# Performance work log

Measured on AMD Instinct MI355X. Metric: run time of the kernel, lower is better.

The kernel has to match this reference:

```python
import jax, jax.numpy as jnp
import numpy as np
from jax import lax

R = 8  # REGION_NUM_

def _avgpool3(x):
    # AvgPool2d(kernel=H-2*(H//3), stride=H//3) -> exactly 3x3 spatial output
    H = x.shape[2]
    s = H // 3
    k = H - 2 * s
    y = lax.reduce_window(x, 0.0, lax.add, (1, 1, k, k), (1, 1, s, s), 'VALID')
    return y / float(k * k)

def _hist_drconv(x, hist, wa, ba, wb, bb, out_ch):
    # x: [B,Cin,H,W], hist: [B,R,H,W]
    B, Cin, H, W = x.shape
    p = _avgpool3(x)                                                     # [B,Cin,3,3]
    h = jax.nn.sigmoid(jnp.einsum('bchw,oc->bohw', p, wa) + ba[None, :, None, None])  # [B,R*R,3,3]
    hg = h.reshape(B, R, R, 3, 3)
    wbg = wb.reshape(R, Cin * out_ch, R)                                 # grouped 1x1 conv, groups=R
    kern = jnp.einsum('brchw,roc->brohw', hg, wbg) + bb.reshape(1, R, Cin * out_ch, 1, 1)
    ki = kern.reshape(B, R * out_ch, Cin, 3, 3)                          # per-sample dynamic kernels
    def per_sample(xi, kb):
        # xi: [Cin,H,W], kb: [R*out,Cin,3,3] -> [R*out,H,W]
        return lax.conv_general_dilated(xi[None], kb, (1, 1), [(1, 1), (1, 1)])[0]
    y = jax.vmap(per_sample)(x, ki)                                      # [B,R*out,H,W]
    y = y.reshape(B, R, out_ch, H, W)
    # asign_index: one-hot of argmax over regions, select-sum
    mask = jax.nn.one_hot(jnp.argmax(hist, axis=1), R, axis=1, dtype=y.dtype)  # [B,R,H,W]
    return (y * mask[:, :, None]).sum(axis=1)                            # [B,out,H,W]

def _bn_relu(y, g, b, m, v):
    scale = (g / jnp.sqrt(v + 1e-5))[None, :, None, None]
    return jax.nn.relu((y - m[None, :, None, None]) * scale + b[None, :, None, None])

def setup_inputs() -> dict:
    key = jax.random.key(0)
    ks = jax.random.split(key, 20)
    B, Cin, Cmid, Cout, H = 8, 8, 8, 8, 256
    f32 = jnp.float32
    d = {}
    d['x'] = jax.random.normal(ks[0], (B, Cin, H, H), f32)
    d['histmap'] = jax.random.uniform(ks[1], (B, R, H, H), dtype=f32)
    d['w1a'] = jax.random.normal(ks[2], (R * R, Cin), f32) * 0.1
    d['b1a'] = jax.random.normal(ks[3], (R * R,), f32) * 0.1
    d['w1b'] = jax.random.normal(ks[4], (R * Cin * Cmid, R), f32) * 0.1
    d['b1b'] = jax.random.normal(ks[5], (R * Cin * Cmid,), f32) * 0.1
    d['g1'] = jax.random.uniform(ks[6], (Cmid,), dtype=f32) + 0.5
    d['be1'] = jax.random.normal(ks[7], (Cmid,), f32) * 0.1
    d['m1'] = jax.random.normal(ks[8], (Cmid,), f32) * 0.1
    d['v1'] = jax.random.uniform(ks[9], (Cmid,), dtype=f32) + 0.5
    d['w2a'] = jax.random.normal(ks[10], (R * R, Cmid), f32) * 0.1
    d['b2a'] = jax.random.normal(ks[11], (R * R,), f32) * 0.1
    d['w2b'] = jax.random.normal(ks[12], (R * Cmid * Cout, R), f32) * 0.1
    d['b2b'] = jax.random.normal(ks[13], (R * Cmid * Cout,), f32) * 0.1
    d['g2'] = jax.random.uniform(ks[14], (Cout,), dtype=f32) + 0.5
    d['be2'] = jax.random.normal(ks[15], (Cout,), f32) * 0.1
    d['m2'] = jax.random.normal(ks[16], (Cout,), f32) * 0.1
    d['v2'] = jax.random.uniform(ks[17], (Cout,), dtype=f32) + 0.5
    return d

def reference(x, histmap, w1a, b1a, w1b, b1b, g1, be1, m1, v1,
              w2a, b2a, w2b, b2b, g2, be2, m2, v2):
    y = _hist_drconv(x, histmap, w1a, b1a, w1b, b1b, 8)
    y = _bn_relu(y, g1, be1, m1, v1)
    y = _hist_drconv(y, histmap, w2a, b2a, w2b, b2b, 8)
    return _bn_relu(y, g2, be2, m2, v2)
```

## Files before the change

### kernel.cpp

```cpp
#include <hip/hip_runtime.h>
#include <math.h>


#define HWPX 65536
#define HDIM 256

typedef __fp16 h2 __attribute__((ext_vector_type(2)));

#if defined(__has_builtin) && __has_builtin(__builtin_amdgcn_fdot2)
__device__ __forceinline__ float fdot2(h2 a, h2 b, float c) {
  return __builtin_amdgcn_fdot2(a, b, c, false);
}
#else
__device__ __forceinline__ float fdot2(h2 a, h2 b, float c) {
  return c + (float)a[0] * (float)b[0] + (float)a[1] * (float)b[1];
}
#endif

union UH { uint u; h2 h; };
union U4H { uint4 u4; h2 h[4]; };

__global__ __launch_bounds__(256) void prep_kernel(const float* __restrict__ x,
                                                   const float* __restrict__ hist,
                                                   float* __restrict__ rs,
                                                   uint* __restrict__ xh,
                                                   unsigned char* __restrict__ regmap) {
  int bid = blockIdx.x;
  int wave = threadIdx.x >> 6, lane = threadIdx.x & 63;
  if (bid < 2048) {
    int cp = bid & 3, rg = (bid >> 2) & 63, b = bid >> 8;
    int row = rg * 4 + wave;
    const float* pa = x + ((size_t)(b * 8 + 2 * cp) * HWPX) + row * HDIM + lane * 4;
    const float4 va = *(const float4*)pa;
    const float4 vb = *(const float4*)(pa + HWPX);
    U4H pk;
    pk.h[0] = __builtin_amdgcn_cvt_pkrtz(va.x, vb.x);
    pk.h[1] = __builtin_amdgcn_cvt_pkrtz(va.y, vb.y);
    pk.h[2] = __builtin_amdgcn_cvt_pkrtz(va.z, vb.z);
    pk.h[3] = __builtin_amdgcn_cvt_pkrtz(va.w, vb.w);
    *(uint4*)(xh + (size_t)(b * 4 + cp) * HWPX + row * HDIM + lane * 4) = pk.u4;
    float a0 = 0.f, a1 = 0.f, a2 = 0.f, b0 = 0.f, b1 = 0.f, b2 = 0.f;
#pragma unroll
    for (int p = 0; p < 4; p++) {
      int px = lane * 4 + p;
      float fa = (&va.x)[p], fb = (&vb.x)[p];
      if (px <= 85)  { a0 += fa; b0 += fb; }
      if (px >= 85 && px <= 170) { a1 += fa; b1 += fb; }
      if (px >= 170) { a2 += fa; b2 += fb; }
    }
#pragma unroll
    for (int off = 32; off >= 1; off >>= 1) {
      a0 += __shfl_xor(a0, off); a1 += __shfl_xor(a1, off); a2 += __shfl_xor(a2, off);
      b0 += __shfl_xor(b0, off); b1 += __shfl_xor(b1, off); b2 += __shfl_xor(b2, off);
    }
    if (lane == 0) {
      float* qa = rs + ((size_t)(b * 8 + 2 * cp) * 256 + row) * 3;
      qa[0] = a0; qa[1] = a1; qa[2] = a2;
      float* qb = qa + 768;
      qb[0] = b0; qb[1] = b1; qb[2] = b2;
    }
  } else {
    int bid2 = bid - 2048;
    int b = bid2 >> 6, rg = bid2 & 63;
    int row = rg * 4 + wave;
    int x0 = lane * 4;
    const float* hp = hist + (size_t)b * 8 * HWPX + row * HDIM + x0;
    float4 hv[8];
#pragma unroll
    for (int r = 0; r < 8; r++) hv[r] = *(const float4*)(hp + (size_t)r * HWPX);
    uchar4 rg4;
#pragma unroll
    for (int p = 0; p < 4; p++) {
      float best = (&hv[0].x)[p];
      int reg = 0;
#pragma unroll
      for (int r = 1; r < 8; r++) {
        float q = (&hv[r].x)[p];
        if (q > best) { best = q; reg = r; }
      }
      (&rg4.x)[p] = (unsigned char)reg;
    }
    *(uchar4*)(regmap + (size_t)b * HWPX + row * HDIM + x0) = rg4;
  }
}

__global__ __launch_bounds__(256) void rowsum_h_kernel(const uint* __restrict__ yh,
                                                       float* __restrict__ rs) {
  int bid = blockIdx.x;
  int cp = bid & 3, rg = (bid >> 2) & 63, b = bid >> 8;
  int wave = threadIdx.x >> 6, lane = threadIdx.x & 63;
  int row = rg * 4 + wave;
  uint4 u = *(const uint4*)(yh + (size_t)(b * 4 + cp) * HWPX + row * HDIM + lane * 4);
  float a0 = 0.f, a1 = 0.f, a2 = 0.f, b0 = 0.f, b1 = 0.f, b2 = 0.f;
#pragma unroll
  for (int p = 0; p < 4; p++) {
    UH w; w.u = (&u.x)[p];
    float fa = (float)w.h[0], fb = (float)w.h[1];
    int px = lane * 4 + p;
    if (px <= 85)  { a0 += fa; b0 += fb; }
    if (px >= 85 && px <= 170) { a1 += fa; b1 += fb; }
    if (px >= 170) { a2 += fa; b2 += fb; }
  }
#pragma unroll
  for (int off = 32; off >= 1; off >>= 1) {
    a0 += __shfl_xor(a0, off); a1 += __shfl_xor(a1, off); a2 += __shfl_xor(a2, off);
    b0 += __shfl_xor(b0, off); b1 += __shfl_xor(b1, off); b2 += __shfl_xor(b2, off);
  }
  if (lane == 0) {
    float* qa = rs + ((size_t)(b * 8 + 2 * cp) * 256 + row) * 3;
    qa[0] = a0; qa[1] = a1; qa[2] = a2;
    float* qb = qa + 768;
    qb[0] = b0; qb[1] = b1; qb[2] = b2;
  }
}

template <int LAYER>
__global__ __launch_bounds__(256) void conv_kernel(
    const uint* __restrict__ xh, const unsigned char* __restrict__ regmap,
    const float* __restrict__ rs,
    const float* __restrict__ wa, const float* __restrict__ ba,
    const float* __restrict__ wb, const float* __restrict__ bb,
    const float* __restrict__ g, const float* __restrict__ be,
    const float* __restrict__ m, const float* __restrict__ v,
    uint* __restrict__ outh, float* __restrict__ outf) {
  __shared__ uint KsU[8 * 292];
  __shared__ float pp[72][3];
  __shared__ float pP[8][9];
  __shared__ float hh[576];
  __shared__ float bns[8], bnsh[8];

  int bid = blockIdx.x;
  int b = bid & 7;
  int rg = bid >> 3;
  int wave = threadIdx.x >> 6, lane = threadIdx.x & 63;
  int row = rg * 4 + wave;
  int x0 = lane * 4;
  int t = threadIdx.x;

  if (t < 216) {
    int u = t / 3, part = t - 3 * (t / 3);
    int c = u / 9, ij = u % 9, i = ij / 3, j = ij % 3;
    int r0 = 85 * i + part * 29;
    int cnt = (part == 2) ? 28 : 29;
    const float* q = rs + ((size_t)(b * 8 + c) * 256 + r0) * 3 + j;
    float s = 0.f;
    for (int k = 0; k < cnt; k++) s += q[k * 3];
    pp[u][part] = s;
  }
  if (t >= 248) {
    int oc = t - 248;
    float s = g[oc] * rsqrtf(v[oc] + 1e-5f);
    bns[oc] = s;
    bnsh[oc] = be[oc] - m[oc] * s;
  }
  __syncthreads();
  if (t < 72) pP[t / 9][t % 9] = (pp[t][0] + pp[t][1] + pp[t][2]) * (1.f / 7396.f);
  __syncthreads();
  for (int u = t; u < 576; u += 256) {
    int o = u / 9, ij = u - o * 9;
    float z = ba[o];
#pragma unroll
    for (int c = 0; c < 8; c++) z += pP[c][ij] * wa[o * 8 + c];
    hh[u] = 1.f / (1.f + expf(-z));
  }
  __syncthreads();
  {
    int reg = t >> 5, z = t & 31, oc = z >> 2, q = z & 3;
    int row0 = reg * 64 + oc * 8 + q * 2;
    const float* w0p = wb + row0 * 8;
    float4 wA  = *(const float4*)(w0p);
    float4 wA2 = *(const float4*)(w0p + 4);
    float4 wB  = *(const float4*)(w0p + 8);
    float4 wB2 = *(const float4*)(w0p + 12);
    float bb0 = bb[row0], bb1 = bb[row0 + 1];
    const float* hp = hh + reg * 72;
#pragma unroll
    for (int tap = 0; tap < 9; tap++) {
      float v0 = bb0, v1 = bb1;
#pragma unroll
      for (int cc = 0; cc < 4; cc++) {
        float hv = hp[cc * 9 + tap];
        v0 += hv * (&wA.x)[cc];
        v1 += hv * (&wB.x)[cc];
      }
#pragma unroll
      for (int cc = 0; cc < 4; cc++) {
        float hv = hp[(4 + cc) * 9 + tap];
        v0 += hv * (&wA2.x)[cc];
        v1 += hv * (&wB2.x)[cc];
      }
      UH pk;
      pk.h[0] = (__fp16)v0;
      pk.h[1] = (__fp16)v1;
      KsU[reg * 292 + tap * 32 + z] = pk.u;
    }
  }
  __syncthreads();

  uint win[4][3][6];
#pragma unroll
  for (int cp = 0; cp < 4; cp++) {
    const uint* plane = xh + (size_t)(b * 4 + cp) * HWPX;
#pragma unroll
    for (int dy = 0; dy < 3; dy++) {
      int yy = row + dy - 1;
      if ((unsigned)yy < 256u) {
        const uint* rp = plane + yy * HDIM + x0;
        uint4 mv = *(const uint4*)rp;
        win[cp][dy][0] = (x0 > 0) ? rp[-1] : 0u;
        win[cp][dy][1] = mv.x; win[cp][dy][2] = mv.y;
        win[cp][dy][3] = mv.z; win[cp][dy][4] = mv.w;
        win[cp][dy][5] = (x0 < 252) ? rp[4] : 0u;
      } else {
#pragma unroll
        for (int q = 0; q < 6; q++) win[cp][dy][q] = 0u;
      }
    }
  }

  uchar4 rg4 = *(const uchar4*)(regmap + (size_t)b * HWPX + row * HDIM + x0);

  float acc[4][8];
#pragma unroll
  for (int p = 0; p < 4; p++)
#pragma unroll
    for (int oc = 0; oc < 8; oc++) acc[p][oc] = 0.f;

#pragma unroll
  for (int p = 0; p < 4; p++) {
    int reg = (&rg4.x)[p];
    const char* Kr = (const char*)KsU + reg * 1168;
#pragma unroll
    for (int di = 0; di < 3; di++) {
#pragma unroll
      for (int dj = 0; dj < 3; dj++) {
        UH w0, w1, w2, w3;
        w0.u = win[0][di][p + dj];
        w1.u = win[1][di][p + dj];
        w2.u = win[2][di][p + dj];
        w3.u = win[3][di][p + dj];
        const char* kt = Kr + (di * 3 + dj) * 128;
#pragma unroll
        for (int oc = 0; oc < 8; oc++) {
          U4H kw;
          kw.u4 = *(const uint4*)(kt + oc * 16);
          float a = acc[p][oc];
          a = fdot2(w0.h, kw.h[0], a);
          a = fdot2(w1.h, kw.h[1], a);
          a = fdot2(w2.h, kw.h[2], a);
          a = fdot2(w3.h, kw.h[3], a);
          acc[p][oc] = a;
        }
      }
    }
  }

#pragma unroll
  for (int p = 0; p < 4; p++)
#pragma unroll
    for (int oc = 0; oc < 8; oc++)
      acc[p][oc] = fmaxf(acc[p][oc] * bns[oc] + bnsh[oc], 0.f);

  if (LAYER == 1) {
#pragma unroll
    for (int cp = 0; cp < 4; cp++) {
      U4H pk;
#pragma unroll
      for (int p = 0; p < 4; p++)
        pk.h[p] = __builtin_amdgcn_cvt_pkrtz(acc[p][2 * cp], acc[p][2 * cp + 1]);
      *(uint4*)(outh + (size_t)(b * 4 + cp) * HWPX + row * HDIM + x0) = pk.u4;
    }
  } else {
#pragma unroll
    for (int oc = 0; oc < 8; oc++) {
      float4 o4 = make_float4(acc[0][oc], acc[1][oc], acc[2][oc], acc[3][oc]);
      *(float4*)(outf + (size_t)(b * 8 + oc) * HWPX + row * HDIM + x0) = o4;
    }
  }
}

extern "C" void kernel_launch(void* const* d_in, const int* in_sizes, int n_in,
                              void* d_out, int out_size, void* d_ws, size_t ws_size,
                              hipStream_t stream) {
  const float* x    = (const float*)d_in[0];
  const float* hist = (const float*)d_in[1];
  const float* w1a  = (const float*)d_in[2];
  const float* b1a  = (const float*)d_in[3];
  const float* w1b  = (const float*)d_in[4];
  const float* b1b  = (const float*)d_in[5];
  const float* g1   = (const float*)d_in[6];
  const float* be1  = (const float*)d_in[7];
  const float* m1   = (const float*)d_in[8];
  const float* v1   = (const float*)d_in[9];
  const float* w2a  = (const float*)d_in[10];
  const float* b2a  = (const float*)d_in[11];
  const float* w2b  = (const float*)d_in[12];
  const float* b2b  = (const float*)d_in[13];
  const float* g2   = (const float*)d_in[14];
  const float* be2  = (const float*)d_in[15];
  const float* m2   = (const float*)d_in[16];
  const float* v2   = (const float*)d_in[17];
  float* outp = (float*)d_out;

  char* ws = (char*)d_ws;
  unsigned char* regmap = (unsigned char*)ws;
  uint* xh  = (uint*)(ws + 524288);
  uint* y1h = (uint*)(ws + 8912896);
  float* rsA = (float*)(ws + 17301504);

  prep_kernel<<<2560, 256, 0, stream>>>(x, hist, rsA, xh, regmap);
  conv_kernel<1><<<512, 256, 0, stream>>>(xh, regmap, rsA, w1a, b1a, w1b, b1b,
                                          g1, be1, m1, v1, y1h, nullptr);
  rowsum_h_kernel<<<2048, 256, 0, stream>>>(y1h, rsA);
  conv_kernel<2><<<512, 256, 0, stream>>>(y1h, regmap, rsA, w2a, b2a, w2b, b2b,
                                          g2, be2, m2, v2, nullptr, outp);
}
```

Measured before the change: 62.28 us.

## Fuse all four stages into one cooperative kernel with grid-wide syncs

Folds prep, layer-1 conv, rowsum and layer-2 conv into a single persistent cooperative kernel of 512 blocks that separates the stages with grid.sync(). This removes three kernel launch boundaries and the drain and refill between them. It uses separate rowsum buffers for the two layers and falls back to the original four launches if the cooperative launch fails. Risks are the cost of grid barriers, the lower occupancy set by launch_bounds(256,2), and prep and rowsum work now spread over fewer blocks that loop.

```diff
diff --git a/kernel.cpp b/kernel.cpp
--- a/kernel.cpp
+++ b/kernel.cpp
@@ -1,5 +1,8 @@
 #include <hip/hip_runtime.h>
+#include <hip/hip_cooperative_groups.h>
 #include <math.h>
+
+namespace cg = cooperative_groups;
 
 
 #define HWPX 65536
@@ -20,15 +23,23 @@
 union UH { uint u; h2 h; };
 union U4H { uint4 u4; h2 h[4]; };
 
-__global__ __launch_bounds__(256) void prep_kernel(const float* __restrict__ x,
-                                                   const float* __restrict__ hist,
-                                                   float* __restrict__ rs,
-                                                   uint* __restrict__ xh,
-                                                   unsigned char* __restrict__ regmap) {
-  int bid = blockIdx.x;
-  int wave = threadIdx.x >> 6, lane = threadIdx.x & 63;
-  if (bid < 2048) {
-    int cp = bid & 3, rg = (bid >> 2) & 63, b = bid >> 8;
+struct ConvSmem {
+  uint KsU[8 * 292];
+  float pp[72][3];
+  float pP[8][9];
+  float hh[576];
+  float bns[8], bnsh[8];
+};
+
+__device__ __forceinline__ void prep_unit(int u, int t,
+                                          const float* __restrict__ x,
+                                          const float* __restrict__ hist,
+                                          float* __restrict__ rs1,
+                                          uint* __restrict__ xh,
+                                          unsigned char* __restrict__ regmap) {
+  int wave = t >> 6, lane = t & 63;
+  if (u < 2048) {
+    int cp = u & 3, rg = (u >> 2) & 63, b = u >> 8;
     int row = rg * 4 + wave;
     const float* pa = x + ((size_t)(b * 8 + 2 * cp) * HWPX) + row * HDIM + lane * 4;
     const float4 va = *(const float4*)pa;
@@ -54,14 +65,14 @@
       b0 += __shfl_xor(b0, off); b1 += __shfl_xor(b1, off); b2 += __shfl_xor(b2, off);
     }
     if (lane == 0) {
-      float* qa = rs + ((size_t)(b * 8 + 2 * cp) * 256 + row) * 3;
+      float* qa = rs1 + ((size_t)(b * 8 + 2 * cp) * 256 + row) * 3;
       qa[0] = a0; qa[1] = a1; qa[2] = a2;
       float* qb = qa + 768;
       qb[0] = b0; qb[1] = b1; qb[2] = b2;
     }
   } else {
-    int bid2 = bid - 2048;
-    int b = bid2 >> 6, rg = bid2 & 63;
+    int u2 = u - 2048;
+    int b = u2 >> 6, rg = u2 & 63;
     int row = rg * 4 + wave;
     int x0 = lane * 4;
     const float* hp = hist + (size_t)b * 8 * HWPX + row * HDIM + x0;
@@ -84,17 +95,17 @@
   }
 }
 
-__global__ __launch_bounds__(256) void rowsum_h_kernel(const uint* __restrict__ yh,
-                                                       float* __restrict__ rs) {
-  int bid = blockIdx.x;
-  int cp = bid & 3, rg = (bid >> 2) & 63, b = bid >> 8;
-  int wave = threadIdx.x >> 6, lane = threadIdx.x & 63;
+__device__ __forceinline__ void rowsum_unit(int u, int t,
+                                            const uint* __restrict__ yh,
+                                            float* __restrict__ rs) {
+  int wave = t >> 6, lane = t & 63;
+  int cp = u & 3, rg = (u >> 2) & 63, b = u >> 8;
   int row = rg * 4 + wave;
-  uint4 u = *(const uint4*)(yh + (size_t)(b * 4 + cp) * HWPX + row * HDIM + lane * 4);
+  uint4 uu = *(const uint4*)(yh + (size_t)(b * 4 + cp) * HWPX + row * HDIM + lane * 4);
   float a0 = 0.f, a1 = 0.f, a2 = 0.f, b0 = 0.f, b1 = 0.f, b2 = 0.f;
 #pragma unroll
   for (int p = 0; p < 4; p++) {
-    UH w; w.u = (&u.x)[p];
+    UH w; w.u = (&uu.x)[p];
     float fa = (float)w.h[0], fb = (float)w.h[1];
     int px = lane * 4 + p;
     if (px <= 85)  { a0 += fa; b0 += fb; }
@@ -115,7 +126,8 @@
 }
 
 template <int LAYER>
-__global__ __launch_bounds__(256) void conv_kernel(
+__device__ __forceinline__ void conv_phase(
+    ConvSmem& sm, int bid, int t,
     const uint* __restrict__ xh, const unsigned char* __restrict__ regmap,
     const float* __restrict__ rs,
     const float* __restrict__ wa, const float* __restrict__ ba,
@@ -123,19 +135,11 @@
     const float* __restrict__ g, const float* __restrict__ be,
     const float* __restrict__ m, const float* __restrict__ v,
     uint* __restrict__ outh, float* __restrict__ outf) {
-  __shared__ uint KsU[8 * 292];
-  __shared__ float pp[72][3];
-  __shared__ float pP[8][9];
-  __shared__ float hh[576];
-  __shared__ float bns[8], bnsh[8];
-
-  int bid = blockIdx.x;
   int b = bid & 7;
   int rg = bid >> 3;
-  int wave = threadIdx.x >> 6, lane = threadIdx.x & 63;
+  int wave = t >> 6, lane = t & 63;
   int row = rg * 4 + wave;
   int x0 = lane * 4;
-  int t = threadIdx.x;
 
   if (t < 216) {
     int u = t / 3, part = t - 3 * (t / 3);
@@ -145,23 +149,23 @@
     const float* q = rs + ((size_t)(b * 8 + c) * 256 + r0) * 3 + j;
     float s = 0.f;
     for (int k = 0; k < cnt; k++) s += q[k * 3];
-    pp[u][part] = s;
+    sm.pp[u][part] = s;
   }
   if (t >= 248) {
     int oc = t - 248;
     float s = g[oc] * rsqrtf(v[oc] + 1e-5f);
-    bns[oc] = s;
-    bnsh[oc] = be[oc] - m[oc] * s;
+    sm.bns[oc] = s;
+    sm.bnsh[oc] = be[oc] - m[oc] * s;
   }
   __syncthreads();
-  if (t < 72) pP[t / 9][t % 9] = (pp[t][0] + pp[t][1] + pp[t][2]) * (1.f / 7396.f);
+  if (t < 72) sm.pP[t / 9][t % 9] = (sm.pp[t][0] + sm.pp[t][1] + sm.pp[t][2]) * (1.f / 7396.f);
   __syncthreads();
   for (int u = t; u < 576; u += 256) {
     int o = u / 9, ij = u - o * 9;
     float z = ba[o];
 #pragma unroll
-    for (int c = 0; c < 8; c++) z += pP[c][ij] * wa[o * 8 + c];
-    hh[u] = 1.f / (1.f + expf(-z));
+    for (int c = 0; c < 8; c++) z += sm.pP[c][ij] * wa[o * 8 + c];
+    sm.hh[u] = 1.f / (1.f + expf(-z));
   }
   __syncthreads();
   {
@@ -173,7 +177,7 @@
     float4 wB  = *(const float4*)(w0p + 8);
     float4 wB2 = *(const float4*)(w0p + 12);
     float bb0 = bb[row0], bb1 = bb[row0 + 1];
-    const float* hp = hh + reg * 72;
+    const float* hp = sm.hh + reg * 72;
 #pragma unroll
     for (int tap = 0; tap < 9; tap++) {
       float v0 = bb0, v1 = bb1;
@@ -192,7 +196,7 @@
       UH pk;
       pk.h[0] = (__fp16)v0;
       pk.h[1] = (__fp16)v1;
-      KsU[reg * 292 + tap * 32 + z] = pk.u;
+      sm.KsU[reg * 292 + tap * 32 + z] = pk.u;
     }
   }
   __syncthreads();
@@ -229,7 +233,7 @@
 #pragma unroll
   for (int p = 0; p < 4; p++) {
     int reg = (&rg4.x)[p];
-    const char* Kr = (const char*)KsU + reg * 1168;
+    const char* Kr = (const char*)sm.KsU + reg * 1168;
 #pragma unroll
     for (int di = 0; di < 3; di++) {
 #pragma unroll
@@ -259,7 +263,7 @@
   for (int p = 0; p < 4; p++)
 #pragma unroll
     for (int oc = 0; oc < 8; oc++)
-      acc[p][oc] = fmaxf(acc[p][oc] * bns[oc] + bnsh[oc], 0.f);
+      acc[p][oc] = fmaxf(acc[p][oc] * sm.bns[oc] + sm.bnsh[oc], 0.f);
 
   if (LAYER == 1) {
 #pragma unroll
@@ -277,6 +281,62 @@
       *(float4*)(outf + (size_t)(b * 8 + oc) * HWPX + row * HDIM + x0) = o4;
     }
   }
+}
+
+__global__ __launch_bounds__(256, 2) void fused_kernel(
+    const float* __restrict__ x, const float* __restrict__ hist,
+    const float* __restrict__ w1a, const float* __restrict__ b1a,
+    const float* __restrict__ w1b, const float* __restrict__ b1b,
+    const float* __restrict__ g1, const float* __restrict__ be1,
+    const float* __restrict__ m1, const float* __restrict__ v1,
+    const float* __restrict__ w2a, const float* __restrict__ b2a,
+    const float* __restrict__ w2b, const float* __restrict__ b2b,
+    const float* __restrict__ g2, const float* __restrict__ be2,
+    const float* __restrict__ m2, const float* __restrict__ v2,
+    float* __restrict__ outp, unsigned char* __restrict__ regmap,
+    uint* __restrict__ xh, uint* __restrict__ y1h,
+    float* __restrict__ rs1, float* __restrict__ rs2) {
+  __shared__ ConvSmem sm;
+  cg::grid_group grid = cg::this_grid();
+  int bid = blockIdx.x;
+  int t = threadIdx.x;
+
+  for (int u = bid; u < 2560; u += 512) prep_unit(u, t, x, hist, rs1, xh, regmap);
+  grid.sync();
+  conv_phase<1>(sm, bid, t, xh, regmap, rs1, w1a, b1a, w1b, b1b,
+                g1, be1, m1, v1, y1h, nullptr);
+  grid.sync();
+  for (int u = bid; u < 2048; u += 512) rowsum_unit(u, t, y1h, rs2);
+  grid.sync();
+  conv_phase<2>(sm, bid, t, y1h, regmap, rs2, w2a, b2a, w2b, b2b,
+                g2, be2, m2, v2, nullptr, outp);
+}
+
+__global__ __launch_bounds__(256) void prep_kernel(const float* __restrict__ x,
+                                                   const float* __restrict__ hist,
+                                                   float* __restrict__ rs,
+                                                   uint* __restrict__ xh,
+                                                   unsigned char* __restrict__ regmap) {
+  prep_unit(blockIdx.x, threadIdx.x, x, hist, rs, xh, regmap);
+}
+
+__global__ __launch_bounds__(256) void rowsum_h_kernel(const uint* __restrict__ yh,
+                                                       float* __restrict__ rs) {
+  rowsum_unit(blockIdx.x, threadIdx.x, yh, rs);
+}
+
+template <int LAYER>
+__global__ __launch_bounds__(256) void conv_kernel(
+    const uint* __restrict__ xh, const unsigned char* __restrict__ regmap,
+    const float* __restrict__ rs,
+    const float* __restrict__ wa, const float* __restrict__ ba,
+    const float* __restrict__ wb, const float* __restrict__ bb,
+    const float* __restrict__ g, const float* __restrict__ be,
+    const float* __restrict__ m, const float* __restrict__ v,
+    uint* __restrict__ outh, float* __restrict__ outf) {
+  __shared__ ConvSmem sm;
+  conv_phase<LAYER>(sm, blockIdx.x, threadIdx.x, xh, regmap, rs,
+                    wa, ba, wb, bb, g, be, m, v, outh, outf);
 }
 
 extern "C" void kernel_launch(void* const* d_in, const int* in_sizes, int n_in,
@@ -306,12 +366,27 @@
   unsigned char* regmap = (unsigned char*)ws;
   uint* xh  = (uint*)(ws + 524288);
   uint* y1h = (uint*)(ws + 8912896);
-  float* rsA = (float*)(ws + 17301504);
-
-  prep_kernel<<<2560, 256, 0, stream>>>(x, hist, rsA, xh, regmap);
-  conv_kernel<1><<<512, 256, 0, stream>>>(xh, regmap, rsA, w1a, b1a, w1b, b1b,
-                                          g1, be1, m1, v1, y1h, nullptr);
-  rowsum_h_kernel<<<2048, 256, 0, stream>>>(y1h, rsA);
-  conv_kernel<2><<<512, 256, 0, stream>>>(y1h, regmap, rsA, w2a, b2a, w2b, b2b,
-                                          g2, be2, m2, v2, nullptr, outp);
-}
+  float* rs1 = (float*)(ws + 17301504);
+  float* rs2 = (float*)(ws + 17399808);
+
+  void* args[] = {
+    (void*)&x, (void*)&hist,
+    (void*)&w1a, (void*)&b1a, (void*)&w1b, (void*)&b1b,
+    (void*)&g1, (void*)&be1, (void*)&m1, (void*)&v1,
+    (void*)&w2a, (void*)&b2a, (void*)&w2b, (void*)&b2b,
+    (void*)&g2, (void*)&be2, (void*)&m2, (void*)&v2,
+    (void*)&outp, (void*)&regmap, (void*)&xh, (void*)&y1h,
+    (void*)&rs1, (void*)&rs2,
+  };
+  hipError_t err = hipLaunchCooperativeKernel((const void*)fused_kernel,
+                                              dim3(512), dim3(256), args, 0, stream);
+  if (err != hipSuccess) {
+    (void)hipGetLastError();
+    prep_kernel<<<2560, 256, 0, stream>>>(x, hist, rs1, xh, regmap);
+    conv_kernel<1><<<512, 256, 0, stream>>>(xh, regmap, rs1, w1a, b1a, w1b, b1b,
+                                            g1, be1, m1, v1, y1h, nullptr);
+    rowsum_h_kernel<<<2048, 256, 0, stream>>>(y1h, rs2);
+    conv_kernel<2><<<512, 256, 0, stream>>>(y1h, regmap, rs2, w2a, b2a, w2b, b2b,
+                                            g2, be2, m2, v2, nullptr, outp);
+  }
+}
```

After: 238.8 us. +283.4%, slower.
